# Performance work log

Hardware: AMD Instinct MI355X
Metric: run time of the kernel (lower is better)

The kernel has to match this reference:

```python
import jax, jax.numpy as jnp
import numpy as np

NUM_CURVE_BINS = 32
NUM_HIST_BINS = 64
W_L1, W_FF, W_LAB, W_MS, W_CURVE, W_HIST, W_WIN = 1.0, 0.3, 0.4, 0.3, 0.4, 0.2, 0.5


def _rgb_to_lab(rgb):
    # rgb: [B,3,H,W] in [0,1]
    M = jnp.array([[0.4124564, 0.3575761, 0.1804375],
                   [0.2126729, 0.7151522, 0.0721750],
                   [0.0193339, 0.1191920, 0.9503041]], dtype=rgb.dtype)
    white = jnp.array([0.95047, 1.0, 1.08883], dtype=rgb.dtype)
    lin = jnp.where(rgb > 0.04045, ((rgb + 0.055) / 1.055) ** 2.4, rgb / 12.92)
    xyz = jnp.einsum('bchw,xc->bxhw', lin, M) / white[None, :, None, None]
    delta = 6.0 / 29.0
    cond = xyz > delta ** 3
    # safe cube root to avoid nan grads at 0 in the unused branch
    f = jnp.where(cond, jnp.maximum(xyz, delta ** 3) ** (1.0 / 3.0),
                  xyz / (3 * delta ** 2) + 4.0 / 29.0)
    L = 116.0 * f[:, 1:2] - 16.0
    a = 500.0 * (f[:, 0:1] - f[:, 1:2])
    b = 200.0 * (f[:, 1:2] - f[:, 2:3])
    return jnp.concatenate([L, a, b], axis=1)


def _avg_pool2(x):
    B, C, H, W = x.shape
    return x.reshape(B, C, H // 2, 2, W // 2, 2).mean(axis=(3, 5))


def _avg_pool11(x):
    # avg_pool2d k=11, stride=1, pad=5, count_include_pad=True
    s = jax.lax.reduce_window(x, 0.0, jax.lax.add, (1, 1, 11, 11), (1, 1, 1, 1),
                              [(0, 0), (0, 0), (5, 5), (5, 5)])
    return s / 121.0


def _soft_hist_cum(x):
    B, C, H, W = x.shape
    centers = jnp.linspace(0.0, 1.0, NUM_HIST_BINS).astype(x.dtype)
    bw = 1.0 / NUM_HIST_BINS
    xf = x.reshape(B, C, H * W, 1)
    w = jnp.exp(-(xf - centers) ** 2 / (2.0 * bw * bw))  # [B,C,HW,bins]
    h = w.sum(axis=2)
    h = h / (h.sum(axis=-1, keepdims=True) + 1e-7)
    return jnp.cumsum(h, axis=-1)


def _hsv_sv(rgb):
    mx = rgb.max(axis=1, keepdims=True)
    mn = rgb.min(axis=1, keepdims=True)
    diff = mx - mn + 1e-7
    return diff / (mx + 1e-7), mx  # (s, v)


def _forward(pred, target, input_img):
    # --- L1 ---
    l1 = jnp.mean(jnp.abs(pred - target))
    # --- Focal frequency (alpha=1, loss_weight=1) ---
    pf = jnp.abs(jnp.fft.rfft2(pred, norm='ortho'))
    tf = jnp.abs(jnp.fft.rfft2(target, norm='ortho'))
    d = jnp.abs(tf - pf)
    w = d / (jnp.mean(d) + 1e-8)
    ff = jnp.mean(w * d)
    # --- LAB perceptual (l_weight=1, ab_weight=2) ---
    pl = _rgb_to_lab(pred)
    tl = _rgb_to_lab(target)
    l_loss = jnp.mean(jnp.abs(pl[:, 0:1] - tl[:, 0:1])) / 100.0
    ab_loss = jnp.mean(jnp.abs(pl[:, 1:3] - tl[:, 1:3])) / 128.0
    lab = 1.0 * l_loss + 2.0 * ab_loss
    # --- Multi-scale ---
    ph, th = _avg_pool2(pred), _avg_pool2(target)
    pq, tq = _avg_pool2(ph), _avg_pool2(th)
    ms = (l1 + jnp.mean(jnp.abs(ph - th)) + jnp.mean(jnp.abs(pq - tq))) / 3.0
    # --- Color curve: per-channel binned means over input_img bins ---
    idx = jnp.clip((input_img * NUM_CURVE_BINS).astype(jnp.int32), 0, NUM_CURVE_BINS - 1)
    seg = (idx + NUM_CURVE_BINS * jnp.arange(3, dtype=jnp.int32)[None, :, None, None]).reshape(-1)
    ns = 3 * NUM_CURVE_BINS
    cnt = jax.ops.segment_sum(jnp.ones(seg.shape, dtype=pred.dtype), seg, num_segments=ns)
    ps = jax.ops.segment_sum(pred.reshape(-1), seg, num_segments=ns)
    ts = jax.ops.segment_sum(target.reshape(-1), seg, num_segments=ns)
    safe_cnt = jnp.maximum(cnt, 1.0)
    pc = jnp.where(cnt > 0, ps / safe_cnt, 0.0)
    tc = jnp.where(cnt > 0, ts / safe_cnt, 0.0)
    curve = jnp.mean(jnp.abs(pc - tc))  # == avg over 3 channels of per-channel bin-mean L1
    # --- Histogram matching (cumulative, EMD approx) ---
    hl = jnp.mean(jnp.abs(_soft_hist_cum(pred) - _soft_hist_cum(target)))
    # --- Window boost ---
    t_s, t_v = _hsv_sv(target)
    mask = ((t_v > 0.6) & (t_s > 0.2)).astype(pred.dtype)
    mask = _avg_pool11(mask)
    wloss = (jnp.abs(pred - target) * mask).sum() / (mask.sum() * 3.0 + 1e-7)
    p_s, _ = _hsv_sv(pred)
    sat = (jnp.abs(p_s - t_s) * mask).sum() / (mask.sum() + 1e-7)
    wb = wloss + 0.5 * sat
    total = (W_L1 * l1 + W_FF * ff + W_LAB * lab + W_MS * ms
             + W_CURVE * curve + W_HIST * hl + W_WIN * wb)
    return total


def setup_inputs() -> dict:
    key = jax.random.key(0)
    k1, k2, k3 = jax.random.split(key, 3)
    shp = (8, 3, 256, 256)
    return {
        'pred': jax.random.uniform(k1, shp, dtype=jnp.float32),
        'target': jax.random.uniform(k2, shp, dtype=jnp.float32),
        'input_img': jax.random.uniform(k3, shp, dtype=jnp.float32),
    }


def reference(pred, target, input_img):
    return _forward(pred, target, input_img)
```

## Files before the change

kernel.cpp:

```cpp
#include <hip/hip_runtime.h>
#include <math.h>

#define HW 65536
#define NPX 524288
#define NEL 1572864

#define P_POINT 4096
#define P_MS    10240
#define P_WIN   11008
#define P_FFT   12544
#define P_CURVE 13360
#define P_HIST  31792
#define MASK_OFF 65536
#define FFT_P   589824
#define FFT_T   (FFT_P + 24*66048)

#define CURVE_SCALE 131072.0f

#define B_POINT 2048
#define B_MS    384
#define B_CURVE 192
#define B_HIST  384
#define B_FFTR  3072
#define G_MEGA1 (B_POINT+B_MS+B_CURVE+B_HIST+B_FFTR)
#define B_WIN   512
#define B_FFTC  408
#define G_MEGA2 (B_WIN+B_FFTC)

__device__ __forceinline__ float fpow24(float x) {
    return __builtin_amdgcn_exp2f(2.4f * __builtin_amdgcn_logf(x));
}
__device__ __forceinline__ float fcbrt(float x) {
    return __builtin_amdgcn_exp2f((1.0f/3.0f) * __builtin_amdgcn_logf(x));
}

__device__ __forceinline__ float labF(float t) {
    return t > 0.008856452f ? fcbrt(t) : t * 7.787037f + 0.13793103f;
}

__device__ __forceinline__ void rgb2lab(float r, float g, float b,
                                        float& L, float& A, float& Bc) {
    float lr = r > 0.04045f ? fpow24((r + 0.055f) * (1.0f/1.055f)) : r * (1.0f/12.92f);
    float lg = g > 0.04045f ? fpow24((g + 0.055f) * (1.0f/1.055f)) : g * (1.0f/12.92f);
    float lb = b > 0.04045f ? fpow24((b + 0.055f) * (1.0f/1.055f)) : b * (1.0f/12.92f);
    float X = (0.4124564f*lr + 0.3575761f*lg + 0.1804375f*lb) * (1.0f/0.95047f);
    float Y = (0.2126729f*lr + 0.7151522f*lg + 0.0721750f*lb);
    float Z = (0.0193339f*lr + 0.1191920f*lg + 0.9503041f*lb) * (1.0f/1.08883f);
    float fx = labF(X), fy = labF(Y), fz = labF(Z);
    L = 116.f*fy - 16.f;
    A = 500.f*(fx - fy);
    Bc = 200.f*(fy - fz);
}

__device__ __forceinline__ float blockSum(float v, float* sb) {
    #pragma unroll
    for (int o = 32; o > 0; o >>= 1) v += __shfl_down(v, o, 64);
    int lane = threadIdx.x & 63, w = threadIdx.x >> 6;
    if (lane == 0) sb[w] = v;
    __syncthreads();
    float r = 0.f;
    if (threadIdx.x == 0) {
        int nw = (blockDim.x + 63) >> 6;
        for (int i = 0; i < nw; ++i) r += sb[i];
    }
    __syncthreads();
    return r;
}

__global__ __launch_bounds__(256) void k_mega1(const float* __restrict__ pred,
                                               const float* __restrict__ targ,
                                               const float* __restrict__ inp,
                                               float* __restrict__ ws) {
    __shared__ __align__(16) unsigned char sm[17408];
    int tid = threadIdx.x;
    int bid = blockIdx.x;

    if (bid < B_POINT) {
        float* sb = (float*)sm;
        int i = bid*256 + tid;
        int b = i >> 16, hw = i & 65535;
        const float* p = pred + b*3*HW + hw;
        const float* t = targ + b*3*HW + hw;
        float pr = p[0], pg = p[HW], pb = p[2*HW];
        float tr = t[0], tg = t[HW], tb = t[2*HW];
        float e3 = fabsf(pr-tr) + fabsf(pg-tg) + fabsf(pb-tb);
        float Lp,Ap,Bp, Lt,At,Bt;
        rgb2lab(pr,pg,pb, Lp,Ap,Bp);
        rgb2lab(tr,tg,tb, Lt,At,Bt);
        float sL = fabsf(Lp-Lt);
        float sab = fabsf(Ap-At) + fabsf(Bp-Bt);
        float tmx = fmaxf(tr, fmaxf(tg, tb)), tmn = fminf(tr, fminf(tg, tb));
        float tsat = (tmx - tmn + 1e-7f) / (tmx + 1e-7f);
        ws[MASK_OFF + i] = (tmx > 0.6f && tsat > 0.2f) ? 1.f : 0.f;
        float v;
        v = blockSum(e3, sb);  if (tid == 0) ws[P_POINT + bid] = v;
        v = blockSum(sL, sb);  if (tid == 0) ws[P_POINT + 2048 + bid] = v;
        v = blockSum(sab, sb); if (tid == 0) ws[P_POINT + 4096 + bid] = v;
    } else if (bid < B_POINT + B_MS) {
        float* sb = (float*)sm;
        int blk = bid - B_POINT;
        int t = blk*256 + tid;
        int sc = t >> 12;
        int q = t & 4095;
        int y4 = q >> 6, x4 = q & 63;
        const float* pp = pred + sc*HW + (y4*4)*256 + x4*4;
        const float* tp = targ + sc*HW + (y4*4)*256 + x4*4;
        float4 p0 = *(const float4*)(pp);
        float4 p1 = *(const float4*)(pp + 256);
        float4 p2 = *(const float4*)(pp + 512);
        float4 p3 = *(const float4*)(pp + 768);
        float4 q0 = *(const float4*)(tp);
        float4 q1 = *(const float4*)(tp + 256);
        float4 q2 = *(const float4*)(tp + 512);
        float4 q3 = *(const float4*)(tp + 768);
        float a00 = (p0.x+p0.y+p1.x+p1.y)*0.25f, a01 = (p0.z+p0.w+p1.z+p1.w)*0.25f;
        float a10 = (p2.x+p2.y+p3.x+p3.y)*0.25f, a11 = (p2.z+p2.w+p3.z+p3.w)*0.25f;
        float b00 = (q0.x+q0.y+q1.x+q1.y)*0.25f, b01 = (q0.z+q0.w+q1.z+q1.w)*0.25f;
        float b10 = (q2.x+q2.y+q3.x+q3.y)*0.25f, b11 = (q2.z+q2.w+q3.z+q3.w)*0.25f;
        float s2 = fabsf(a00-b00)+fabsf(a01-b01)+fabsf(a10-b10)+fabsf(a11-b11);
        float s4 = fabsf((a00+a01+a10+a11)*0.25f - (b00+b01+b10+b11)*0.25f);
        float v;
        v = blockSum(s2, sb); if (tid == 0) ws[P_MS + blk] = v;
        v = blockSum(s4, sb); if (tid == 0) ws[P_MS + 384 + blk] = v;
    } else if (bid < B_POINT + B_MS + B_CURVE) {
        unsigned* h = (unsigned*)sm;
        if (tid < 256) h[tid] = 0u;
        if (tid < 32) h[256 + tid] = 0u;
        __syncthreads();
        int blk = bid - (B_POINT + B_MS);
        int slice = blk >> 3, part = blk & 7;
        int c = slice % 3;
        int base = slice * HW + part * 8192;
        const float4* ip = (const float4*)(inp + base);
        const float4* pp = (const float4*)(pred + base);
        const float4* tp = (const float4*)(targ + base);
        int segbase = 32 * c;
        #pragma unroll
        for (int it = 0; it < 8; ++it) {
            float4 a = ip[it*256 + tid];
            float4 p = pp[it*256 + tid];
            float4 t = tp[it*256 + tid];
            float av[4] = {a.x, a.y, a.z, a.w};
            float pv[4] = {p.x, p.y, p.z, p.w};
            float tv[4] = {t.x, t.y, t.z, t.w};
            #pragma unroll
            for (int j = 0; j < 4; ++j) {
                int idx = (int)(av[j] * 32.f);
                idx = min(max(idx, 0), 31);
                unsigned s3 = (unsigned)((segbase + idx) * 3);
                atomicAdd(&h[s3],     1u);
                atomicAdd(&h[s3 + 1], (unsigned)__float2uint_rn(pv[j] * CURVE_SCALE));
                atomicAdd(&h[s3 + 2], (unsigned)__float2uint_rn(tv[j] * CURVE_SCALE));
            }
        }
        __syncthreads();
        if (tid < 96) {
            unsigned v = h[segbase*3 + tid];
            int q = tid - (tid/3)*3;
            float f = (q == 0) ? (float)v : (float)v * (1.f/CURVE_SCALE);
            ws[P_CURVE + blk*96 + tid] = f;
        }
    } else if (bid < B_POINT + B_MS + B_CURVE + B_HIST) {
        unsigned (*fh)[1024] = (unsigned(*)[1024])sm;
        float* wtab = (float*)(sm + 16384);
        int hb = bid - (B_POINT + B_MS + B_CURVE);
        int s = hb >> 3, part = hb & 7;
        const float* src = (s < 24 ? pred + s*HW : targ + (s-24)*HW) + part*8192;
        #pragma unroll
        for (int j = 0; j < 16; ++j) ((unsigned*)sm)[tid + 256*j] = 0u;
        if (tid < 193) {
            float d = (float)(tid - 96);
            wtab[tid] = __builtin_amdgcn_exp2f(-0.002907957f * d * d);
        }
        __syncthreads();
        int wv = tid >> 6;
        const float4* s4 = (const float4*)src;
        #pragma unroll
        for (int it = 0; it < 8; ++it) {
            float4 v = s4[it*256 + tid];
            float vals[4] = {v.x, v.y, v.z, v.w};
            #pragma unroll
            for (int e = 0; e < 4; ++e) {
                unsigned f = __float2uint_rn(vals[e] * 1008.f);
                f = min(f, 1008u);
                atomicAdd(&fh[wv][f], 1u);
            }
        }
        __syncthreads();
        #pragma unroll
        for (int j = 0; j < 4; ++j) {
            int idx = tid + 256*j;
            fh[0][idx] = fh[0][idx] + fh[1][idx] + fh[2][idx] + fh[3][idx];
        }
        __syncthreads();
        int k = tid >> 2, q = tid & 3;
        float acc = 0.f;
        for (int i = q; i < 193; i += 4) {
            int f = 16*k + i - 96;
            if (f >= 0 && f <= 1008) acc += (float)fh[0][f] * wtab[i];
        }
        acc += __shfl_xor(acc, 1, 64);
        acc += __shfl_xor(acc, 2, 64);
        if (q == 0) ws[P_HIST + hb*64 + k] = acc;
    } else {
        float2 (*a4)[256] = (float2(*)[256])sm;
        int fb = bid - (B_POINT + B_MS + B_CURVE + B_HIST);
        int fid = tid >> 6, l = tid & 63;
        int R = fb*4 + fid;
        int s = R >> 8, r = R & 255;
        const float* src = (s < 24 ? pred + s*HW : targ + (s-24)*HW) + r*256;
        float2* out = (float2*)(ws + (s < 24 ? FFT_P + s*66048 : FFT_T + (s-24)*66048)) + r*129;
        float2* a = a4[fid];
        #pragma unroll
        for (int j = 0; j < 4; ++j) {
            int i = l + 64*j;
            a[__brev((unsigned)i) >> 24] = make_float2(src[i], 0.f);
        }
        __syncthreads();
        #pragma unroll
        for (int st = 0; st < 8; ++st) {
            int half = 1 << st, m = half << 1;
            #pragma unroll
            for (int kk = 0; kk < 2; ++kk) {
                int bb = l + 64*kk;
                int j = bb & (half - 1);
                int i0 = ((bb >> st) << (st + 1)) + j;
                int i1 = i0 + half;
                float ang = -6.283185307f * (float)j / (float)m;
                float si, co;
                __sincosf(ang, &si, &co);
                float2 u = a[i0], v = a[i1];
                float2 w = make_float2(v.x*co - v.y*si, v.x*si + v.y*co);
                a[i0] = make_float2(u.x + w.x, u.y + w.y);
                a[i1] = make_float2(u.x - w.x, u.y - w.y);
            }
            __syncthreads();
        }
        out[l] = a[l];
        out[l + 64] = a[l + 64];
        if (l == 0) out[128] = a[128];
    }
}

__global__ __launch_bounds__(256) void k_mega2(const float* __restrict__ pred,
                                               const float* __restrict__ targ,
                                               float* __restrict__ ws) {
    __shared__ __align__(16) unsigned char sm[33024];
    int tid = threadIdx.x;
    int bid = blockIdx.x;

    if (bid < B_WIN) {
        float (*msk)[256] = (float(*)[256])sm;
        float (*hs)[256]  = (float(*)[256])(sm + 14336);
        float* sb = (float*)(sm + 28672);
        int b = bid >> 6, strip = bid & 63;
        int y0 = strip * 4;
        int x = tid;
        const float* mbase = ws + MASK_OFF + b*HW;
        #pragma unroll
        for (int r = 0; r < 14; ++r) {
            int yy = y0 - 5 + r;
            msk[r][x] = (yy >= 0 && yy < 256) ? mbase[yy*256 + x] : 0.f;
        }
        __syncthreads();
        #pragma unroll
        for (int r = 0; r < 14; ++r) {
            float hsum = 0.f;
            #pragma unroll
            for (int dx = -5; dx <= 5; ++dx) {
                int xx = x + dx;
                if (xx >= 0 && xx < 256) hsum += msk[r][xx];
            }
            hs[r][x] = hsum;
        }
        __syncthreads();
        float acc_e3 = 0.f, acc_sd = 0.f, acc_m = 0.f;
        #pragma unroll
        for (int j = 0; j < 4; ++j) {
            int ry = y0 + j;
            float vs = 0.f;
            #pragma unroll
            for (int dy = 0; dy < 11; ++dy) vs += hs[j + dy][x];
            float m = vs * (1.f/121.f);
            const float* p = pred + b*3*HW + ry*256 + x;
            const float* t = targ + b*3*HW + ry*256 + x;
            float pr = p[0], pg = p[HW], pb = p[2*HW];
            float tr = t[0], tg = t[HW], tb = t[2*HW];
            float e3 = fabsf(pr-tr) + fabsf(pg-tg) + fabsf(pb-tb);
            float tmx = fmaxf(tr, fmaxf(tg, tb)), tmn = fminf(tr, fminf(tg, tb));
            float tsat = (tmx - tmn + 1e-7f) / (tmx + 1e-7f);
            float pmx = fmaxf(pr, fmaxf(pg, pb)), pmn = fminf(pr, fminf(pg, pb));
            float psat = (pmx - pmn + 1e-7f) / (pmx + 1e-7f);
            acc_e3 += e3 * m;
            acc_sd += fabsf(psat - tsat) * m;
            acc_m  += m;
        }
        float v;
        v = blockSum(acc_e3, sb); if (tid == 0) ws[P_WIN + bid] = v;
        v = blockSum(acc_sd, sb); if (tid == 0) ws[P_WIN + 512 + bid] = v;
        v = blockSum(acc_m,  sb); if (tid == 0) ws[P_WIN + 1024 + bid] = v;
    } else {
        float2 (*arr)[257] = (float2(*)[257])sm;
        float* sb = (float*)(sm + 32896);
        int cb = bid - B_WIN;
        int s = cb / 17, kt = cb - s*17;
        int k0 = kt * 8;
        const float2* srcP = (const float2*)(ws + FFT_P) + s*33024;
        const float2* srcT = (const float2*)(ws + FFT_T) + s*33024;
        int kk = tid & 7, r0 = tid >> 3;
        int col = k0 + kk;
        bool valid = (col <= 128);
        #pragma unroll
        for (int rb = 0; rb < 8; ++rb) {
            int r = r0 + rb*32;
            int br = __brev((unsigned)r) >> 24;
            float2 vp = valid ? srcP[r*129 + col] : make_float2(0.f, 0.f);
            arr[kk][br] = vp;
            float2 vt = valid ? srcT[r*129 + col] : make_float2(0.f, 0.f);
            arr[8 + kk][br] = vt;
        }
        __syncthreads();
        int fid = tid >> 4, w = tid & 15;
        float2* a = arr[fid];
        #pragma unroll
        for (int st = 0; st < 8; ++st) {
            int half = 1 << st, m = half << 1;
            #pragma unroll
            for (int q = 0; q < 8; ++q) {
                int bb = w + (q << 4);
                int j = bb & (half - 1);
                int i0 = ((bb >> st) << (st + 1)) + j;
                int i1 = i0 + half;
                float ang = -6.283185307f * (float)j / (float)m;
                float si, co;
                __sincosf(ang, &si, &co);
                float2 u = a[i0], v = a[i1];
                float2 wv = make_float2(v.x*co - v.y*si, v.x*si + v.y*co);
                a[i0] = make_float2(u.x + wv.x, u.y + wv.y);
                a[i1] = make_float2(u.x - wv.x, u.y - wv.y);
            }
            __syncthreads();
        }
        float d1 = 0.f, d2 = 0.f;
        #pragma unroll
        for (int e = 0; e < 8; ++e) {
            int idx = tid + e*256;
            int k = idx >> 8, r = idx & 255;
            if (k0 + k <= 128) {
                float2 zp = arr[k][r], zt = arr[8 + k][r];
                float mp = sqrtf(zp.x*zp.x + zp.y*zp.y);
                float mt = sqrtf(zt.x*zt.x + zt.y*zt.y);
                float d = fabsf(mt - mp) * (1.f/256.f);
                d1 += d; d2 += d*d;
            }
        }
        float v;
        v = blockSum(d1, sb); if (tid == 0) ws[P_FFT + cb] = v;
        v = blockSum(d2, sb); if (tid == 0) ws[P_FFT + 408 + cb] = v;
    }
}

__global__ __launch_bounds__(256) void k_final(const float* __restrict__ ws,
                                               float* __restrict__ out) {
    __shared__ float shist[3072];
    __shared__ float red[256];
    __shared__ float sb[8];
    int tid = threadIdx.x;
    for (int q = tid; q < 3072; q += 256) {
        int s = q >> 6, k = q & 63;
        float t = 0.f;
        const float* base = ws + P_HIST + s*8*64 + k;
        #pragma unroll
        for (int p = 0; p < 8; ++p) t += base[p*64];
        shist[q] = t;
    }
    float a0=0.f, a1=0.f, a2=0.f;
    for (int i = tid; i < 2048; i += 256) {
        a0 += ws[P_POINT + i];
        a1 += ws[P_POINT + 2048 + i];
        a2 += ws[P_POINT + 4096 + i];
    }
    float w0=0.f, w1=0.f, w2=0.f;
    for (int i = tid; i < 512; i += 256) {
        w0 += ws[P_WIN + i];
        w1 += ws[P_WIN + 512 + i];
        w2 += ws[P_WIN + 1024 + i];
    }
    float m0=0.f, m1=0.f;
    for (int i = tid; i < 384; i += 256) {
        m0 += ws[P_MS + i];
        m1 += ws[P_MS + 384 + i];
    }
    float f0=0.f, f1=0.f;
    for (int i = tid; i < 408; i += 256) {
        f0 += ws[P_FFT + i];
        f1 += ws[P_FFT + 408 + i];
    }
    float sum_e3 = blockSum(a0, sb);
    float sum_L  = blockSum(a1, sb);
    float sum_ab = blockSum(a2, sb);
    float wnum   = blockSum(w0, sb);
    float wsat   = blockSum(w1, sb);
    float wm     = blockSum(w2, sb);
    float S2     = blockSum(m0, sb);
    float S4     = blockSum(m1, sb);
    float d1     = blockSum(f0, sb);
    float d2     = blockSum(f1, sb);
    __syncthreads();
    float cv = 0.f;
    if (tid < 96) {
        int c = tid >> 5, i = tid & 31;
        float cnt=0.f, ps=0.f, ts=0.f;
        for (int ss = c; ss < 24; ss += 3) {
            for (int p = 0; p < 8; ++p) {
                const float* base = ws + P_CURVE + ((ss<<3) + p)*96 + i*3;
                cnt += base[0]; ps += base[1]; ts += base[2];
            }
        }
        if (cnt > 0.f) cv = fabsf(ps - ts) / cnt;
    }
    red[tid] = cv;
    __syncthreads();
    for (int o = 128; o > 0; o >>= 1) { if (tid < o) red[tid] += red[tid + o]; __syncthreads(); }
    float curve = red[0] / 96.f;
    __syncthreads();
    float hacc = 0.f;
    if (tid < 24) {
        const float* hp = shist + tid*64;
        const float* ht = shist + (24 + tid)*64;
        float sp = 0.f, stt = 0.f;
        for (int k = 0; k < 64; ++k) { sp += hp[k]; stt += ht[k]; }
        float ip = 1.f / (sp + 1e-7f), it = 1.f / (stt + 1e-7f);
        float cp = 0.f, ct = 0.f;
        for (int k = 0; k < 64; ++k) {
            cp += hp[k] * ip;
            ct += ht[k] * it;
            hacc += fabsf(cp - ct);
        }
    }
    red[tid] = hacc;
    __syncthreads();
    for (int o = 128; o > 0; o >>= 1) { if (tid < o) red[tid] += red[tid + o]; __syncthreads(); }
    float hl = red[0] / 1536.f;
    if (tid == 0) {
        float l1  = sum_e3 / (float)NEL;
        float lab = (sum_L / (float)NPX) * 0.01f + 2.f * (sum_ab / (2.f * (float)NPX * 128.f));
        float ms  = (l1 + S2 / 393216.f + S4 / 98304.f) * (1.f/3.f);
        const float M = 792576.f;
        float ff  = (d2 / M) / (d1 / M + 1e-8f);
        float wb  = wnum / (wm*3.f + 1e-7f) + 0.5f * (wsat / (wm + 1e-7f));
        out[0] = l1 + 0.3f*ff + 0.4f*lab + 0.3f*ms + 0.4f*curve + 0.2f*hl + 0.5f*wb;
    }
}

extern "C" void kernel_launch(void* const* d_in, const int* in_sizes, int n_in,
                              void* d_out, int out_size, void* d_ws, size_t ws_size,
                              hipStream_t stream) {
    const float* pred = (const float*)d_in[0];
    const float* targ = (const float*)d_in[1];
    const float* inp  = (const float*)d_in[2];
    float* ws = (float*)d_ws;
    float* out = (float*)d_out;

    k_mega1<<<G_MEGA1, 256, 0, stream>>>(pred, targ, inp, ws);
    k_mega2<<<G_MEGA2, 256, 0, stream>>>(pred, targ, ws);
    k_final<<<1,       256, 0, stream>>>(ws, out);
}
```

Before: 69.28 us.

## Pack two real rows per complex FFT, use DIF with SoA, fuse final reduction

```diff
diff --git a/kernel.cpp b/kernel.cpp
--- a/kernel.cpp
+++ b/kernel.cpp
@@ -5,6 +5,7 @@
 #define NPX 524288
 #define NEL 1572864
 
+#define LB_CNT  4000
 #define P_POINT 4096
 #define P_MS    10240
 #define P_WIN   11008
@@ -21,7 +22,7 @@
 #define B_MS    384
 #define B_CURVE 192
 #define B_HIST  384
-#define B_FFTR  3072
+#define B_FFTR  1536
 #define G_MEGA1 (B_POINT+B_MS+B_CURVE+B_HIST+B_FFTR)
 #define B_WIN   512
 #define B_FFTC  408
@@ -33,11 +34,9 @@
 __device__ __forceinline__ float fcbrt(float x) {
     return __builtin_amdgcn_exp2f((1.0f/3.0f) * __builtin_amdgcn_logf(x));
 }
-
 __device__ __forceinline__ float labF(float t) {
     return t > 0.008856452f ? fcbrt(t) : t * 7.787037f + 0.13793103f;
 }
-
 __device__ __forceinline__ void rgb2lab(float r, float g, float b,
                                         float& L, float& A, float& Bc) {
     float lr = r > 0.04045f ? fpow24((r + 0.055f) * (1.0f/1.055f)) : r * (1.0f/12.92f);
@@ -76,6 +75,7 @@
     int bid = blockIdx.x;
 
     if (bid < B_POINT) {
+        if (bid == 0 && tid == 0) *((unsigned*)(ws + LB_CNT)) = 0u;
         float* sb = (float*)sm;
         int i = bid*256 + tid;
         int b = i >> 16, hw = i & 65535;
@@ -203,49 +203,72 @@
         acc += __shfl_xor(acc, 2, 64);
         if (q == 0) ws[P_HIST + hb*64 + k] = acc;
     } else {
-        float2 (*a4)[256] = (float2(*)[256])sm;
+        float (*re4)[256] = (float(*)[256])sm;
+        float (*im4)[256] = (float(*)[256])(sm + 4096);
         int fb = bid - (B_POINT + B_MS + B_CURVE + B_HIST);
         int fid = tid >> 6, l = tid & 63;
-        int R = fb*4 + fid;
-        int s = R >> 8, r = R & 255;
-        const float* src = (s < 24 ? pred + s*HW : targ + (s-24)*HW) + r*256;
-        float2* out = (float2*)(ws + (s < 24 ? FFT_P + s*66048 : FFT_T + (s-24)*66048)) + r*129;
-        float2* a = a4[fid];
+        int g = fb*4 + fid;
+        int s = g >> 7, pr = g & 127;
+        const float* src = (s < 24 ? pred + s*HW : targ + (s-24)*HW) + (2*pr)*256;
+        float* re = re4[fid];
+        float* im = im4[fid];
         #pragma unroll
         for (int j = 0; j < 4; ++j) {
-            int i = l + 64*j;
-            a[__brev((unsigned)i) >> 24] = make_float2(src[i], 0.f);
+            int x = l + 64*j;
+            re[x] = src[x];
+            im[x] = src[256 + x];
         }
         __syncthreads();
         #pragma unroll
         for (int st = 0; st < 8; ++st) {
-            int half = 1 << st, m = half << 1;
+            int m = 256 >> st, half = m >> 1, sh = 7 - st;
             #pragma unroll
             for (int kk = 0; kk < 2; ++kk) {
                 int bb = l + 64*kk;
                 int j = bb & (half - 1);
-                int i0 = ((bb >> st) << (st + 1)) + j;
+                int i0 = ((bb >> sh) << (sh + 1)) + j;
                 int i1 = i0 + half;
                 float ang = -6.283185307f * (float)j / (float)m;
                 float si, co;
                 __sincosf(ang, &si, &co);
-                float2 u = a[i0], v = a[i1];
-                float2 w = make_float2(v.x*co - v.y*si, v.x*si + v.y*co);
-                a[i0] = make_float2(u.x + w.x, u.y + w.y);
-                a[i1] = make_float2(u.x - w.x, u.y - w.y);
+                float ur = re[i0], ui = im[i0];
+                float vr = re[i1], vi = im[i1];
+                re[i0] = ur + vr;
+                im[i0] = ui + vi;
+                float dr = ur - vr, di = ui - vi;
+                re[i1] = dr*co - di*si;
+                im[i1] = dr*si + di*co;
             }
             __syncthreads();
         }
-        out[l] = a[l];
-        out[l + 64] = a[l + 64];
-        if (l == 0) out[128] = a[128];
+        float2* outbase = (float2*)(ws + (s < 24 ? FFT_P + s*66048 : FFT_T + (s-24)*66048));
+        float2* outA = outbase + (2*pr)*129;
+        float2* outB = outbase + (2*pr+1)*129;
+        #pragma unroll
+        for (int kk = 0; kk < 2; ++kk) {
+            int k = l + 64*kk;
+            int kb  = __brev((unsigned)k) >> 24;
+            int kmb = __brev((unsigned)((256 - k) & 255)) >> 24;
+            float zr = re[kb], zi = im[kb];
+            float wr = re[kmb], wi = im[kmb];
+            outA[k] = make_float2(0.5f*(zr + wr), 0.5f*(zi - wi));
+            outB[k] = make_float2(0.5f*(zi + wi), 0.5f*(wr - zr));
+        }
+        if (l == 0) {
+            int kb = __brev(128u) >> 24;
+            float zr = re[kb], zi = im[kb];
+            outA[128] = make_float2(zr, 0.f);
+            outB[128] = make_float2(zi, 0.f);
+        }
     }
 }
 
 __global__ __launch_bounds__(256) void k_mega2(const float* __restrict__ pred,
                                                const float* __restrict__ targ,
-                                               float* __restrict__ ws) {
+                                               float* __restrict__ ws,
+                                               float* __restrict__ out) {
     __shared__ __align__(16) unsigned char sm[33024];
+    __shared__ unsigned lastFlag;
     int tid = threadIdx.x;
     int bid = blockIdx.x;
 
@@ -300,7 +323,8 @@
         v = blockSum(acc_sd, sb); if (tid == 0) ws[P_WIN + 512 + bid] = v;
         v = blockSum(acc_m,  sb); if (tid == 0) ws[P_WIN + 1024 + bid] = v;
     } else {
-        float2 (*arr)[257] = (float2(*)[257])sm;
+        float (*re_)[257] = (float(*)[257])sm;
+        float (*im_)[257] = (float(*)[257])(sm + 16448);
         float* sb = (float*)(sm + 32896);
         int cb = bid - B_WIN;
         int s = cb / 17, kt = cb - s*17;
@@ -313,31 +337,34 @@
         #pragma unroll
         for (int rb = 0; rb < 8; ++rb) {
             int r = r0 + rb*32;
-            int br = __brev((unsigned)r) >> 24;
             float2 vp = valid ? srcP[r*129 + col] : make_float2(0.f, 0.f);
-            arr[kk][br] = vp;
+            re_[kk][r] = vp.x; im_[kk][r] = vp.y;
             float2 vt = valid ? srcT[r*129 + col] : make_float2(0.f, 0.f);
-            arr[8 + kk][br] = vt;
+            re_[8 + kk][r] = vt.x; im_[8 + kk][r] = vt.y;
         }
         __syncthreads();
         int fid = tid >> 4, w = tid & 15;
-        float2* a = arr[fid];
+        float* re = re_[fid];
+        float* im = im_[fid];
         #pragma unroll
         for (int st = 0; st < 8; ++st) {
-            int half = 1 << st, m = half << 1;
+            int m = 256 >> st, half = m >> 1, sh = 7 - st;
             #pragma unroll
             for (int q = 0; q < 8; ++q) {
                 int bb = w + (q << 4);
                 int j = bb & (half - 1);
-                int i0 = ((bb >> st) << (st + 1)) + j;
+                int i0 = ((bb >> sh) << (sh + 1)) + j;
                 int i1 = i0 + half;
                 float ang = -6.283185307f * (float)j / (float)m;
                 float si, co;
                 __sincosf(ang, &si, &co);
-                float2 u = a[i0], v = a[i1];
-                float2 wv = make_float2(v.x*co - v.y*si, v.x*si + v.y*co);
-                a[i0] = make_float2(u.x + wv.x, u.y + wv.y);
-                a[i1] = make_float2(u.x - wv.x, u.y - wv.y);
+                float ur = re[i0], ui = im[i0];
+                float vr = re[i1], vi = im[i1];
+                re[i0] = ur + vr;
+                im[i0] = ui + vi;
+                float dr = ur - vr, di = ui - vi;
+                re[i1] = dr*co - di*si;
+                im[i1] = dr*si + di*co;
             }
             __syncthreads();
         }
@@ -347,10 +374,9 @@
             int idx = tid + e*256;
             int k = idx >> 8, r = idx & 255;
             if (k0 + k <= 128) {
-                float2 zp = arr[k][r], zt = arr[8 + k][r];
-                float mp = sqrtf(zp.x*zp.x + zp.y*zp.y);
-                float mt = sqrtf(zt.x*zt.x + zt.y*zt.y);
-                float d = fabsf(mt - mp) * (1.f/256.f);
+                float pr2 = re_[k][r]*re_[k][r] + im_[k][r]*im_[k][r];
+                float tr2 = re_[8+k][r]*re_[8+k][r] + im_[8+k][r]*im_[8+k][r];
+                float d = fabsf(sqrtf(tr2) - sqrtf(pr2)) * (1.f/256.f);
                 d1 += d; d2 += d*d;
             }
         }
@@ -358,98 +384,102 @@
         v = blockSum(d1, sb); if (tid == 0) ws[P_FFT + cb] = v;
         v = blockSum(d2, sb); if (tid == 0) ws[P_FFT + 408 + cb] = v;
     }
-}
-
-__global__ __launch_bounds__(256) void k_final(const float* __restrict__ ws,
-                                               float* __restrict__ out) {
-    __shared__ float shist[3072];
-    __shared__ float red[256];
-    __shared__ float sb[8];
-    int tid = threadIdx.x;
-    for (int q = tid; q < 3072; q += 256) {
-        int s = q >> 6, k = q & 63;
-        float t = 0.f;
-        const float* base = ws + P_HIST + s*8*64 + k;
-        #pragma unroll
-        for (int p = 0; p < 8; ++p) t += base[p*64];
-        shist[q] = t;
-    }
-    float a0=0.f, a1=0.f, a2=0.f;
-    for (int i = tid; i < 2048; i += 256) {
-        a0 += ws[P_POINT + i];
-        a1 += ws[P_POINT + 2048 + i];
-        a2 += ws[P_POINT + 4096 + i];
-    }
-    float w0=0.f, w1=0.f, w2=0.f;
-    for (int i = tid; i < 512; i += 256) {
-        w0 += ws[P_WIN + i];
-        w1 += ws[P_WIN + 512 + i];
-        w2 += ws[P_WIN + 1024 + i];
-    }
-    float m0=0.f, m1=0.f;
-    for (int i = tid; i < 384; i += 256) {
-        m0 += ws[P_MS + i];
-        m1 += ws[P_MS + 384 + i];
-    }
-    float f0=0.f, f1=0.f;
-    for (int i = tid; i < 408; i += 256) {
-        f0 += ws[P_FFT + i];
-        f1 += ws[P_FFT + 408 + i];
-    }
-    float sum_e3 = blockSum(a0, sb);
-    float sum_L  = blockSum(a1, sb);
-    float sum_ab = blockSum(a2, sb);
-    float wnum   = blockSum(w0, sb);
-    float wsat   = blockSum(w1, sb);
-    float wm     = blockSum(w2, sb);
-    float S2     = blockSum(m0, sb);
-    float S4     = blockSum(m1, sb);
-    float d1     = blockSum(f0, sb);
-    float d2     = blockSum(f1, sb);
+
+    __threadfence();
+    if (tid == 0)
+        lastFlag = (atomicAdd((unsigned*)(ws + LB_CNT), 1u) == (unsigned)(G_MEGA2 - 1)) ? 1u : 0u;
     __syncthreads();
-    float cv = 0.f;
-    if (tid < 96) {
-        int c = tid >> 5, i = tid & 31;
-        float cnt=0.f, ps=0.f, ts=0.f;
-        for (int ss = c; ss < 24; ss += 3) {
-            for (int p = 0; p < 8; ++p) {
-                const float* base = ws + P_CURVE + ((ss<<3) + p)*96 + i*3;
-                cnt += base[0]; ps += base[1]; ts += base[2];
-            }
-        }
-        if (cnt > 0.f) cv = fabsf(ps - ts) / cnt;
-    }
-    red[tid] = cv;
-    __syncthreads();
-    for (int o = 128; o > 0; o >>= 1) { if (tid < o) red[tid] += red[tid + o]; __syncthreads(); }
-    float curve = red[0] / 96.f;
-    __syncthreads();
-    float hacc = 0.f;
-    if (tid < 24) {
-        const float* hp = shist + tid*64;
-        const float* ht = shist + (24 + tid)*64;
-        float sp = 0.f, stt = 0.f;
-        for (int k = 0; k < 64; ++k) { sp += hp[k]; stt += ht[k]; }
-        float ip = 1.f / (sp + 1e-7f), it = 1.f / (stt + 1e-7f);
-        float cp = 0.f, ct = 0.f;
-        for (int k = 0; k < 64; ++k) {
-            cp += hp[k] * ip;
-            ct += ht[k] * it;
-            hacc += fabsf(cp - ct);
-        }
-    }
-    red[tid] = hacc;
-    __syncthreads();
-    for (int o = 128; o > 0; o >>= 1) { if (tid < o) red[tid] += red[tid + o]; __syncthreads(); }
-    float hl = red[0] / 1536.f;
-    if (tid == 0) {
-        float l1  = sum_e3 / (float)NEL;
-        float lab = (sum_L / (float)NPX) * 0.01f + 2.f * (sum_ab / (2.f * (float)NPX * 128.f));
-        float ms  = (l1 + S2 / 393216.f + S4 / 98304.f) * (1.f/3.f);
-        const float M = 792576.f;
-        float ff  = (d2 / M) / (d1 / M + 1e-8f);
-        float wb  = wnum / (wm*3.f + 1e-7f) + 0.5f * (wsat / (wm + 1e-7f));
-        out[0] = l1 + 0.3f*ff + 0.4f*lab + 0.3f*ms + 0.4f*curve + 0.2f*hl + 0.5f*wb;
+    if (lastFlag) {
+        __threadfence();
+        float* shist = (float*)sm;
+        float* red   = (float*)(sm + 12288);
+        float* sb    = (float*)(sm + 13312);
+        for (int q = tid; q < 3072; q += 256) {
+            int s = q >> 6, k = q & 63;
+            float t = 0.f;
+            const float* base = ws + P_HIST + s*8*64 + k;
+            #pragma unroll
+            for (int p = 0; p < 8; ++p) t += base[p*64];
+            shist[q] = t;
+        }
+        float a0=0.f, a1=0.f, a2=0.f;
+        for (int i = tid; i < 2048; i += 256) {
+            a0 += ws[P_POINT + i];
+            a1 += ws[P_POINT + 2048 + i];
+            a2 += ws[P_POINT + 4096 + i];
+        }
+        float w0=0.f, w1=0.f, w2=0.f;
+        for (int i = tid; i < 512; i += 256) {
+            w0 += ws[P_WIN + i];
+            w1 += ws[P_WIN + 512 + i];
+            w2 += ws[P_WIN + 1024 + i];
+        }
+        float m0=0.f, m1=0.f;
+        for (int i = tid; i < 384; i += 256) {
+            m0 += ws[P_MS + i];
+            m1 += ws[P_MS + 384 + i];
+        }
+        float f0=0.f, f1=0.f;
+        for (int i = tid; i < 408; i += 256) {
+            f0 += ws[P_FFT + i];
+            f1 += ws[P_FFT + 408 + i];
+        }
+        __syncthreads();
+        float sum_e3 = blockSum(a0, sb);
+        float sum_L  = blockSum(a1, sb);
+        float sum_ab = blockSum(a2, sb);
+        float wnum   = blockSum(w0, sb);
+        float wsat   = blockSum(w1, sb);
+        float wm     = blockSum(w2, sb);
+        float S2     = blockSum(m0, sb);
+        float S4     = blockSum(m1, sb);
+        float d1     = blockSum(f0, sb);
+        float d2     = blockSum(f1, sb);
+        __syncthreads();
+        float cv = 0.f;
+        if (tid < 96) {
+            int c = tid >> 5, i = tid & 31;
+            float cnt=0.f, ps=0.f, ts=0.f;
+            for (int ss = c; ss < 24; ss += 3) {
+                for (int p = 0; p < 8; ++p) {
+                    const float* base = ws + P_CURVE + ((ss<<3) + p)*96 + i*3;
+                    cnt += base[0]; ps += base[1]; ts += base[2];
+                }
+            }
+            if (cnt > 0.f) cv = fabsf(ps - ts) / cnt;
+        }
+        red[tid] = cv;
+        __syncthreads();
+        for (int o = 128; o > 0; o >>= 1) { if (tid < o) red[tid] += red[tid + o]; __syncthreads(); }
+        float curve = red[0] / 96.f;
+        __syncthreads();
+        float hacc = 0.f;
+        if (tid < 24) {
+            const float* hp = shist + tid*64;
+            const float* ht = shist + (24 + tid)*64;
+            float sp = 0.f, stt = 0.f;
+            for (int k = 0; k < 64; ++k) { sp += hp[k]; stt += ht[k]; }
+            float ip = 1.f / (sp + 1e-7f), it = 1.f / (stt + 1e-7f);
+            float cp = 0.f, ct = 0.f;
+            for (int k = 0; k < 64; ++k) {
+                cp += hp[k] * ip;
+                ct += ht[k] * it;
+                hacc += fabsf(cp - ct);
+            }
+        }
+        red[tid] = hacc;
+        __syncthreads();
+        for (int o = 128; o > 0; o >>= 1) { if (tid < o) red[tid] += red[tid + o]; __syncthreads(); }
+        float hl = red[0] / 1536.f;
+        if (tid == 0) {
+            float l1  = sum_e3 / (float)NEL;
+            float lab = (sum_L / (float)NPX) * 0.01f + 2.f * (sum_ab / (2.f * (float)NPX * 128.f));
+            float ms  = (l1 + S2 / 393216.f + S4 / 98304.f) * (1.f/3.f);
+            const float M = 792576.f;
+            float ff  = (d2 / M) / (d1 / M + 1e-8f);
+            float wb  = wnum / (wm*3.f + 1e-7f) + 0.5f * (wsat / (wm + 1e-7f));
+            out[0] = l1 + 0.3f*ff + 0.4f*lab + 0.3f*ms + 0.4f*curve + 0.2f*hl + 0.5f*wb;
+        }
     }
 }
 
@@ -463,6 +493,5 @@
     float* out = (float*)d_out;
 
     k_mega1<<<G_MEGA1, 256, 0, stream>>>(pred, targ, inp, ws);
-    k_mega2<<<G_MEGA2, 256, 0, stream>>>(pred, targ, ws);
-    k_final<<<1,       256, 0, stream>>>(ws, out);
-}
+    k_mega2<<<G_MEGA2, 256, 0, stream>>>(pred, targ, ws, out);
+}
```

Result: slower. 129.8 us (+87.3%).
